# Kernel tuning notes

Hardware: AMD Instinct MI355X
Metric: run time of the kernel (lower is better)

## Reference

```python
import jax, jax.numpy as jnp
import numpy as np

NUM_HEADS = 16


def setup_inputs() -> dict:
    key = jax.random.key(0)
    ks = jax.random.split(key, 7)
    B_, N, C = 512, 64, 512
    x = jax.random.normal(ks[0], (B_, N, C), dtype=jnp.float32)
    attn_bias = jax.random.normal(ks[1], (NUM_HEADS, N, N), dtype=jnp.float32)
    mask = jax.random.normal(ks[2], (B_, N, N), dtype=jnp.float32)
    qkv_w = jax.random.normal(ks[3], (3 * C, C), dtype=jnp.float32) * (C ** -0.5)
    qkv_b = jax.random.normal(ks[4], (3 * C,), dtype=jnp.float32) * 0.02
    proj_w = jax.random.normal(ks[5], (C, C), dtype=jnp.float32) * (C ** -0.5)
    proj_b = jax.random.normal(ks[6], (C,), dtype=jnp.float32) * 0.02
    return {"x": x, "attn_bias": attn_bias, "mask": mask,
            "qkv_w": qkv_w, "qkv_b": qkv_b, "proj_w": proj_w, "proj_b": proj_b}


def reference(x, attn_bias, mask, qkv_w, qkv_b, proj_w, proj_b):
    B_, N, C = x.shape
    H = NUM_HEADS
    hd = C // H
    scale = hd ** -0.5
    # qkv projection: (B_, N, 3, H, hd) -> (3, B_, H, N, hd)
    qkv = (x @ qkv_w.T + qkv_b).reshape(B_, N, 3, H, hd)
    qkv = jnp.transpose(qkv, (2, 0, 3, 1, 4))
    q, k, v = qkv[0], qkv[1], qkv[2]
    attn = jnp.einsum('bhnd,bhmd->bhnm', q * scale, k)  # (B_, H, N, N)
    attn = attn + attn_bias            # (H, N, N) broadcasts over batch
    attn = attn + mask[:, None]        # (B_, 1, N, N)
    attn = jax.nn.softmax(attn, axis=-1)
    out = jnp.einsum('bhnm,bhmd->bhnd', attn, v)
    out = jnp.transpose(out, (0, 2, 1, 3)).reshape(B_, N, C)
    return out @ proj_w.T + proj_b
```

## Files before the change

kernel.cpp:

```cpp
#include <hip/hip_runtime.h>
#include <stdint.h>

typedef __attribute__((ext_vector_type(8))) __bf16 bf16x8;
typedef __attribute__((ext_vector_type(4))) float f32x4;
typedef __attribute__((ext_vector_type(4))) float fl4;
typedef __attribute__((ext_vector_type(8))) unsigned short us8;
typedef __attribute__((ext_vector_type(4))) unsigned short us4;

__device__ __forceinline__ unsigned short f2bf(float f) {
  union { float f; unsigned int u; } v;
  v.f = f;
  unsigned int r = v.u + 0x7FFFu + ((v.u >> 16) & 1u);
  return (unsigned short)(r >> 16);
}

#define GLOAD_LDS16(g, l)                                                   \
  __builtin_amdgcn_global_load_lds(                                         \
      (const __attribute__((address_space(1))) void*)(g),                   \
      (__attribute__((address_space(3))) void*)(l), 16, 0, 0)

__global__ void convert_all_kernel(const float* __restrict__ x,
                                   const float* __restrict__ wq,
                                   const float* __restrict__ wp,
                                   unsigned short* __restrict__ ox,
                                   unsigned short* __restrict__ owq,
                                   unsigned short* __restrict__ owp) {
  const int i = (blockIdx.x * blockDim.x + threadIdx.x) * 4;
  const float* src;
  unsigned short* dst;
  int off;
  if (i < 16777216) {
    src = x; dst = ox; off = i;
  } else if (i < 17563648) {
    src = wq; dst = owq; off = i - 16777216;
  } else {
    src = wp; dst = owp; off = i - 17563648;
  }
  fl4 v = *(const fl4*)(src + off);
  us4 o;
  o[0] = f2bf(v[0]);
  o[1] = f2bf(v[1]);
  o[2] = f2bf(v[2]);
  o[3] = f2bf(v[3]);
  *(us4*)(dst + off) = o;
}

template <bool OUT_BF16>
__global__ __launch_bounds__(512, 4) void gemm128_kernel(
    const unsigned short* __restrict__ A, const unsigned short* __restrict__ B,
    const float* __restrict__ bias, void* __restrict__ Cout, int M, int N,
    int K, int NT) {
  __shared__ __align__(16) unsigned short lds[32768];
  char* base = (char*)lds;

  const int tid = threadIdx.x;
  const int lane = tid & 63;
  const int wid = tid >> 6;
  const int lr = lane & 15;
  const int lg = lane >> 4;
  const int wm = wid >> 2;
  const int wn = wid & 3;

  const int bid = blockIdx.x;
  const int bm = ((bid & 31) + (bid / (32 * NT)) * 32) << 7;
  const int bn = (((bid >> 5) % NT)) << 7;

  const int srow = tid >> 3;
  const int scsw = ((tid & 7) << 4) ^ ((srow & 7) << 4);
  const char* Ag = (const char*)A;
  const char* Bg = (const char*)B;
  const size_t Kb = (size_t)K * 2;

#define STAGE(kt, p)                                                           \
  {                                                                            \
    char* la_ = base + (p)*32768;                                              \
    char* lb_ = la_ + 16384;                                                   \
    _Pragma("unroll") for (int i_ = 0; i_ < 2; ++i_) {                         \
      GLOAD_LDS16(Ag + (size_t)(bm + srow + i_ * 64) * Kb + (kt)*128 + scsw,   \
                  la_ + (srow + i_ * 64) * 128 + (tid & 7) * 16);              \
      GLOAD_LDS16(Bg + (size_t)(bn + srow + i_ * 64) * Kb + (kt)*128 + scsw,   \
                  lb_ + (srow + i_ * 64) * 128 + (tid & 7) * 16);              \
    }                                                                          \
  }

  const int swz = (lr & 7) << 4;
  const int ck0 = (lg << 4) ^ swz;
  const int ck1 = (64 + (lg << 4)) ^ swz;

  f32x4 acc[4][2];
#pragma unroll
  for (int m = 0; m < 4; ++m)
#pragma unroll
    for (int n = 0; n < 2; ++n) acc[m][n] = (f32x4){0.f, 0.f, 0.f, 0.f};

  const int nkt = K >> 6;

  STAGE(0, 0);
  __syncthreads();

  for (int kt = 0; kt < nkt; ++kt) {
    const int p = kt & 1;
    if (kt + 1 < nkt) STAGE(kt + 1, p ^ 1);

    const char* la = base + p * 32768;
    const char* lb = la + 16384;
    bf16x8 af[4][2], bfr[2][2];
#pragma unroll
    for (int m = 0; m < 4; ++m) {
      const int arow = (wm * 64 + m * 16 + lr) << 7;
      af[m][0] = *(const bf16x8*)(la + arow + ck0);
      af[m][1] = *(const bf16x8*)(la + arow + ck1);
    }
#pragma unroll
    for (int n = 0; n < 2; ++n) {
      const int brow = (wn * 32 + n * 16 + lr) << 7;
      bfr[n][0] = *(const bf16x8*)(lb + brow + ck0);
      bfr[n][1] = *(const bf16x8*)(lb + brow + ck1);
    }
#pragma unroll
    for (int kk = 0; kk < 2; ++kk)
#pragma unroll
      for (int m = 0; m < 4; ++m)
#pragma unroll
        for (int n = 0; n < 2; ++n)
          acc[m][n] = __builtin_amdgcn_mfma_f32_16x16x32_bf16(
              af[m][kk], bfr[n][kk], acc[m][n], 0, 0, 0);
    __syncthreads();
  }
#undef STAGE

  const int crow0 = bm + wm * 64 + lg * 4;
  const int ccol0 = bn + wn * 32 + lr;
#pragma unroll
  for (int n = 0; n < 2; ++n) {
    const int col = ccol0 + n * 16;
    const float bv = bias[col];
#pragma unroll
    for (int m = 0; m < 4; ++m) {
#pragma unroll
      for (int j = 0; j < 4; ++j) {
        const int row = crow0 + m * 16 + j;
        const float val = acc[m][n][j] + bv;
        if (OUT_BF16)
          ((unsigned short*)Cout)[(size_t)row * N + col] = f2bf(val);
        else
          ((float*)Cout)[(size_t)row * N + col] = val;
      }
    }
  }
}

__global__ __launch_bounds__(256, 4) void attn_kernel(
    const unsigned short* __restrict__ qkv, const float* __restrict__ abias,
    const float* __restrict__ mask, unsigned short* __restrict__ out) {
  __shared__ __align__(16) unsigned short lq[64 * 40];
  __shared__ __align__(16) unsigned short lk[64 * 40];
  __shared__ __align__(16) unsigned short lvT[32 * 72];
  __shared__ __align__(16) unsigned short lp[64 * 72];

  const int bid = blockIdx.x;
  const int id2 = (bid & 7) * 1024 + (bid >> 3);
  const int b = id2 >> 4;
  const int h = id2 & 15;
  const int tid = threadIdx.x;
  const int lane = tid & 63;
  const int wid = tid >> 6;
  const int lr = lane & 15;
  const int lg = lane >> 4;
  const int lk8 = lg * 8;

  {
    const int r = tid >> 2;
    const int d0 = (tid & 3) * 8;
    const size_t bse = (size_t)(b * 64 + r) * 1536 + h * 32 + d0;
    us8 qv = *(const us8*)(qkv + bse);
    us8 kv = *(const us8*)(qkv + bse + 512);
    us8 vv = *(const us8*)(qkv + bse + 1024);
    *(us8*)(lq + r * 40 + d0) = qv;
    *(us8*)(lk + r * 40 + d0) = kv;
#pragma unroll
    for (int i = 0; i < 8; ++i) lvT[(d0 + i) * 72 + r] = vv[i];
  }
  __syncthreads();

  f32x4 s[4];
  {
    bf16x8 aq = *(const bf16x8*)(lq + (wid * 16 + lr) * 40 + lk8);
#pragma unroll
    for (int n = 0; n < 4; ++n) {
      bf16x8 bk = *(const bf16x8*)(lk + (n * 16 + lr) * 40 + lk8);
      f32x4 z = {0.f, 0.f, 0.f, 0.f};
      s[n] = __builtin_amdgcn_mfma_f32_16x16x32_bf16(aq, bk, z, 0, 0, 0);
    }
  }
  const float scale = 0.17677669529663687f;
  const int row0 = wid * 16 + lg * 4;
#pragma unroll
  for (int j = 0; j < 4; ++j) {
    const int row = row0 + j;
    const float* ab = abias + (h * 64 + row) * 64 + lr;
    const float* mk = mask + ((size_t)b * 64 + row) * 64 + lr;
#pragma unroll
    for (int n = 0; n < 4; ++n)
      s[n][j] = s[n][j] * scale + ab[n * 16] + mk[n * 16];
  }

  float mx[4], sm[4];
#pragma unroll
  for (int j = 0; j < 4; ++j)
    mx[j] = fmaxf(fmaxf(s[0][j], s[1][j]), fmaxf(s[2][j], s[3][j]));
#pragma unroll
  for (int xm = 1; xm <= 8; xm <<= 1)
#pragma unroll
    for (int j = 0; j < 4; ++j) mx[j] = fmaxf(mx[j], __shfl_xor(mx[j], xm));
#pragma unroll
  for (int j = 0; j < 4; ++j) sm[j] = 0.f;
#pragma unroll
  for (int n = 0; n < 4; ++n)
#pragma unroll
    for (int j = 0; j < 4; ++j) {
      const float e = __expf(s[n][j] - mx[j]);
      s[n][j] = e;
      sm[j] += e;
    }
#pragma unroll
  for (int xm = 1; xm <= 8; xm <<= 1)
#pragma unroll
    for (int j = 0; j < 4; ++j) sm[j] += __shfl_xor(sm[j], xm);
#pragma unroll
  for (int j = 0; j < 4; ++j) sm[j] = 1.f / sm[j];
#pragma unroll
  for (int n = 0; n < 4; ++n)
#pragma unroll
    for (int j = 0; j < 4; ++j)
      lp[(row0 + j) * 72 + n * 16 + lr] = f2bf(s[n][j] * sm[j]);
  __syncthreads();

  f32x4 o[2];
  o[0] = (f32x4){0.f, 0.f, 0.f, 0.f};
  o[1] = o[0];
#pragma unroll
  for (int kk = 0; kk < 2; ++kk) {
    bf16x8 pa = *(const bf16x8*)(lp + (wid * 16 + lr) * 72 + kk * 32 + lk8);
#pragma unroll
    for (int d = 0; d < 2; ++d) {
      bf16x8 vb = *(const bf16x8*)(lvT + (d * 16 + lr) * 72 + kk * 32 + lk8);
      o[d] = __builtin_amdgcn_mfma_f32_16x16x32_bf16(pa, vb, o[d], 0, 0, 0);
    }
  }
#pragma unroll
  for (int d = 0; d < 2; ++d) {
    const int col = h * 32 + d * 16 + lr;
#pragma unroll
    for (int j = 0; j < 4; ++j) {
      const int row = row0 + j;
      out[(size_t)(b * 64 + row) * 512 + col] = f2bf(o[d][j]);
    }
  }
}

extern "C" void kernel_launch(void* const* d_in, const int* in_sizes, int n_in,
                              void* d_out, int out_size, void* d_ws,
                              size_t ws_size, hipStream_t stream) {
  (void)in_sizes; (void)n_in; (void)out_size; (void)ws_size;
  const float* x = (const float*)d_in[0];
  const float* abias = (const float*)d_in[1];
  const float* mask = (const float*)d_in[2];
  const float* qkv_w = (const float*)d_in[3];
  const float* qkv_b = (const float*)d_in[4];
  const float* proj_w = (const float*)d_in[5];
  const float* proj_b = (const float*)d_in[6];

  char* ws = (char*)d_ws;
  unsigned short* ws_x = (unsigned short*)(ws);
  unsigned short* ws_qkv = (unsigned short*)(ws + 33554432);
  unsigned short* ws_wq = (unsigned short*)(ws + 134217728);
  unsigned short* ws_wp = (unsigned short*)(ws + 135790592);
  unsigned short* ws_att = ws_x;

  convert_all_kernel<<<17408, 256, 0, stream>>>(x, qkv_w, proj_w, ws_x, ws_wq,
                                                ws_wp);

  gemm128_kernel<true><<<3072, 512, 0, stream>>>(ws_x, ws_wq, qkv_b, ws_qkv,
                                                 32768, 1536, 512, 12);

  attn_kernel<<<8192, 256, 0, stream>>>(ws_qkv, abias, mask, ws_att);

  gemm128_kernel<false><<<1024, 512, 0, stream>>>(ws_att, ws_wp, proj_b, d_out,
                                                  32768, 512, 512, 4);
}
```

Before: 259.9 us.

## Widen GEMM tiles to 128x256 with a triple-buffered async LDS pipeline

```diff
diff --git a/kernel.cpp b/kernel.cpp
--- a/kernel.cpp
+++ b/kernel.cpp
@@ -46,11 +46,11 @@
 }
 
 template <bool OUT_BF16>
-__global__ __launch_bounds__(512, 4) void gemm128_kernel(
+__global__ __launch_bounds__(512, 2) void gemm_k3_kernel(
     const unsigned short* __restrict__ A, const unsigned short* __restrict__ B,
     const float* __restrict__ bias, void* __restrict__ Cout, int M, int N,
     int K, int NT) {
-  __shared__ __align__(16) unsigned short lds[32768];
+  __shared__ __align__(16) unsigned short lds[73728];
   char* base = (char*)lds;
 
   const int tid = threadIdx.x;
@@ -63,7 +63,7 @@
 
   const int bid = blockIdx.x;
   const int bm = ((bid & 31) + (bid / (32 * NT)) * 32) << 7;
-  const int bn = (((bid >> 5) % NT)) << 7;
+  const int bn = ((bid >> 5) % NT) << 8;
 
   const int srow = tid >> 3;
   const int scsw = ((tid & 7) << 4) ^ ((srow & 7) << 4);
@@ -71,15 +71,17 @@
   const char* Bg = (const char*)B;
   const size_t Kb = (size_t)K * 2;
 
-#define STAGE(kt, p)                                                           \
+#define STAGE(kt)                                                              \
   {                                                                            \
-    char* la_ = base + (p)*32768;                                              \
+    char* la_ = base + ((kt) % 3) * 49152;                                     \
     char* lb_ = la_ + 16384;                                                   \
     _Pragma("unroll") for (int i_ = 0; i_ < 2; ++i_) {                         \
       GLOAD_LDS16(Ag + (size_t)(bm + srow + i_ * 64) * Kb + (kt)*128 + scsw,   \
-                  la_ + (srow + i_ * 64) * 128 + (tid & 7) * 16);              \
-      GLOAD_LDS16(Bg + (size_t)(bn + srow + i_ * 64) * Kb + (kt)*128 + scsw,   \
-                  lb_ + (srow + i_ * 64) * 128 + (tid & 7) * 16);              \
+                  la_ + (tid + i_ * 512) * 16);                                \
+    }                                                                          \
+    _Pragma("unroll") for (int j_ = 0; j_ < 4; ++j_) {                         \
+      GLOAD_LDS16(Bg + (size_t)(bn + srow + j_ * 64) * Kb + (kt)*128 + scsw,   \
+                  lb_ + (tid + j_ * 512) * 16);                                \
     }                                                                          \
   }
 
@@ -87,24 +89,29 @@
   const int ck0 = (lg << 4) ^ swz;
   const int ck1 = (64 + (lg << 4)) ^ swz;
 
-  f32x4 acc[4][2];
+  f32x4 acc[4][4];
 #pragma unroll
   for (int m = 0; m < 4; ++m)
 #pragma unroll
-    for (int n = 0; n < 2; ++n) acc[m][n] = (f32x4){0.f, 0.f, 0.f, 0.f};
+    for (int n = 0; n < 4; ++n) acc[m][n] = (f32x4){0.f, 0.f, 0.f, 0.f};
 
   const int nkt = K >> 6;
 
-  STAGE(0, 0);
-  __syncthreads();
+  STAGE(0);
+  STAGE(1);
 
   for (int kt = 0; kt < nkt; ++kt) {
-    const int p = kt & 1;
-    if (kt + 1 < nkt) STAGE(kt + 1, p ^ 1);
-
-    const char* la = base + p * 32768;
+    if (kt + 1 < nkt)
+      asm volatile("s_waitcnt vmcnt(6)" ::: "memory");
+    else
+      asm volatile("s_waitcnt vmcnt(0)" ::: "memory");
+    __builtin_amdgcn_s_barrier();
+    asm volatile("" ::: "memory");
+    if (kt + 2 < nkt) STAGE(kt + 2);
+
+    const char* la = base + (kt % 3) * 49152;
     const char* lb = la + 16384;
-    bf16x8 af[4][2], bfr[2][2];
+    bf16x8 af[4][2], bfr[4][2];
 #pragma unroll
     for (int m = 0; m < 4; ++m) {
       const int arow = (wm * 64 + m * 16 + lr) << 7;
@@ -112,8 +119,8 @@
       af[m][1] = *(const bf16x8*)(la + arow + ck1);
     }
 #pragma unroll
-    for (int n = 0; n < 2; ++n) {
-      const int brow = (wn * 32 + n * 16 + lr) << 7;
+    for (int n = 0; n < 4; ++n) {
+      const int brow = (wn * 64 + n * 16 + lr) << 7;
       bfr[n][0] = *(const bf16x8*)(lb + brow + ck0);
       bfr[n][1] = *(const bf16x8*)(lb + brow + ck1);
     }
@@ -122,17 +129,18 @@
 #pragma unroll
       for (int m = 0; m < 4; ++m)
 #pragma unroll
-        for (int n = 0; n < 2; ++n)
+        for (int n = 0; n < 4; ++n)
           acc[m][n] = __builtin_amdgcn_mfma_f32_16x16x32_bf16(
               af[m][kk], bfr[n][kk], acc[m][n], 0, 0, 0);
-    __syncthreads();
+    asm volatile("s_waitcnt lgkmcnt(0)" ::: "memory");
+    __builtin_amdgcn_sched_barrier(0);
   }
 #undef STAGE
 
   const int crow0 = bm + wm * 64 + lg * 4;
-  const int ccol0 = bn + wn * 32 + lr;
-#pragma unroll
-  for (int n = 0; n < 2; ++n) {
+  const int ccol0 = bn + wn * 64 + lr;
+#pragma unroll
+  for (int n = 0; n < 4; ++n) {
     const int col = ccol0 + n * 16;
     const float bv = bias[col];
 #pragma unroll
@@ -281,11 +289,11 @@
   convert_all_kernel<<<17408, 256, 0, stream>>>(x, qkv_w, proj_w, ws_x, ws_wq,
                                                 ws_wp);
 
-  gemm128_kernel<true><<<3072, 512, 0, stream>>>(ws_x, ws_wq, qkv_b, ws_qkv,
-                                                 32768, 1536, 512, 12);
+  gemm_k3_kernel<true><<<1536, 512, 0, stream>>>(ws_x, ws_wq, qkv_b, ws_qkv,
+                                                 32768, 1536, 512, 6);
 
   attn_kernel<<<8192, 256, 0, stream>>>(ws_qkv, abias, mask, ws_att);
 
-  gemm128_kernel<false><<<1024, 512, 0, stream>>>(ws_att, ws_wp, proj_b, d_out,
-                                                  32768, 512, 512, 4);
-}
+  gemm_k3_kernel<false><<<512, 512, 0, stream>>>(ws_att, ws_wp, proj_b, d_out,
+                                                 32768, 512, 512, 2);
+}
```

After: 268.5 us. +3.3%, slower.

## Process four heads per attention block with double-buffered prefetch; grid-stride bf16 conversion

Applied to the files above, without the earlier changes.

```diff
diff --git a/kernel.cpp b/kernel.cpp
--- a/kernel.cpp
+++ b/kernel.cpp
@@ -25,24 +25,27 @@
                                    unsigned short* __restrict__ ox,
                                    unsigned short* __restrict__ owq,
                                    unsigned short* __restrict__ owp) {
-  const int i = (blockIdx.x * blockDim.x + threadIdx.x) * 4;
-  const float* src;
-  unsigned short* dst;
-  int off;
-  if (i < 16777216) {
-    src = x; dst = ox; off = i;
-  } else if (i < 17563648) {
-    src = wq; dst = owq; off = i - 16777216;
-  } else {
-    src = wp; dst = owp; off = i - 17563648;
-  }
-  fl4 v = *(const fl4*)(src + off);
-  us4 o;
-  o[0] = f2bf(v[0]);
-  o[1] = f2bf(v[1]);
-  o[2] = f2bf(v[2]);
-  o[3] = f2bf(v[3]);
-  *(us4*)(dst + off) = o;
+  const int NCH = 2228224;
+  const int stride = gridDim.x * blockDim.x;
+  for (int c = blockIdx.x * blockDim.x + threadIdx.x; c < NCH; c += stride) {
+    const int i = c * 8;
+    const float* src;
+    unsigned short* dst;
+    int off;
+    if (i < 16777216) {
+      src = x; dst = ox; off = i;
+    } else if (i < 17563648) {
+      src = wq; dst = owq; off = i - 16777216;
+    } else {
+      src = wp; dst = owp; off = i - 17563648;
+    }
+    fl4 v0 = *(const fl4*)(src + off);
+    fl4 v1 = *(const fl4*)(src + off + 4);
+    us8 o;
+    o[0] = f2bf(v0[0]); o[1] = f2bf(v0[1]); o[2] = f2bf(v0[2]); o[3] = f2bf(v0[3]);
+    o[4] = f2bf(v1[0]); o[5] = f2bf(v1[1]); o[6] = f2bf(v1[2]); o[7] = f2bf(v1[3]);
+    *(us8*)(dst + off) = o;
+  }
 }
 
 template <bool OUT_BF16>
@@ -153,109 +156,136 @@
 __global__ __launch_bounds__(256, 4) void attn_kernel(
     const unsigned short* __restrict__ qkv, const float* __restrict__ abias,
     const float* __restrict__ mask, unsigned short* __restrict__ out) {
-  __shared__ __align__(16) unsigned short lq[64 * 40];
-  __shared__ __align__(16) unsigned short lk[64 * 40];
-  __shared__ __align__(16) unsigned short lvT[32 * 72];
+  __shared__ __align__(16) unsigned short bufs[2][7424];
   __shared__ __align__(16) unsigned short lp[64 * 72];
 
   const int bid = blockIdx.x;
-  const int id2 = (bid & 7) * 1024 + (bid >> 3);
-  const int b = id2 >> 4;
-  const int h = id2 & 15;
+  const int id2 = (bid & 7) * 256 + (bid >> 3);
+  const int b = id2 >> 2;
+  const int hq = (id2 & 3) << 2;
   const int tid = threadIdx.x;
   const int lane = tid & 63;
   const int wid = tid >> 6;
   const int lr = lane & 15;
   const int lg = lane >> 4;
   const int lk8 = lg * 8;
-
+  const int row0 = wid * 16 + lg * 4;
+  const float scale = 0.17677669529663687f;
+
+  const int sr = tid >> 2;
+  const int sd0 = (tid & 3) * 8;
+  const size_t sbase = (size_t)(b * 64 + sr) * 1536 + sd0;
+
+  us8 qv, kv, vv;
   {
-    const int r = tid >> 2;
-    const int d0 = (tid & 3) * 8;
-    const size_t bse = (size_t)(b * 64 + r) * 1536 + h * 32 + d0;
-    us8 qv = *(const us8*)(qkv + bse);
-    us8 kv = *(const us8*)(qkv + bse + 512);
-    us8 vv = *(const us8*)(qkv + bse + 1024);
-    *(us8*)(lq + r * 40 + d0) = qv;
-    *(us8*)(lk + r * 40 + d0) = kv;
-#pragma unroll
-    for (int i = 0; i < 8; ++i) lvT[(d0 + i) * 72 + r] = vv[i];
+    const unsigned short* p = qkv + sbase + hq * 32;
+    qv = *(const us8*)(p);
+    kv = *(const us8*)(p + 512);
+    vv = *(const us8*)(p + 1024);
+  }
+  {
+    unsigned short* d0b = bufs[0];
+    *(us8*)(d0b + sr * 40 + sd0) = qv;
+    *(us8*)(d0b + 2560 + sr * 40 + sd0) = kv;
+#pragma unroll
+    for (int i = 0; i < 8; ++i) d0b[5120 + (sd0 + i) * 72 + sr] = vv[i];
   }
   __syncthreads();
 
-  f32x4 s[4];
-  {
-    bf16x8 aq = *(const bf16x8*)(lq + (wid * 16 + lr) * 40 + lk8);
-#pragma unroll
-    for (int n = 0; n < 4; ++n) {
-      bf16x8 bk = *(const bf16x8*)(lk + (n * 16 + lr) * 40 + lk8);
-      f32x4 z = {0.f, 0.f, 0.f, 0.f};
-      s[n] = __builtin_amdgcn_mfma_f32_16x16x32_bf16(aq, bk, z, 0, 0, 0);
-    }
-  }
-  const float scale = 0.17677669529663687f;
-  const int row0 = wid * 16 + lg * 4;
-#pragma unroll
-  for (int j = 0; j < 4; ++j) {
-    const int row = row0 + j;
-    const float* ab = abias + (h * 64 + row) * 64 + lr;
-    const float* mk = mask + ((size_t)b * 64 + row) * 64 + lr;
-#pragma unroll
-    for (int n = 0; n < 4; ++n)
-      s[n][j] = s[n][j] * scale + ab[n * 16] + mk[n * 16];
-  }
-
-  float mx[4], sm[4];
-#pragma unroll
-  for (int j = 0; j < 4; ++j)
-    mx[j] = fmaxf(fmaxf(s[0][j], s[1][j]), fmaxf(s[2][j], s[3][j]));
-#pragma unroll
-  for (int xm = 1; xm <= 8; xm <<= 1)
-#pragma unroll
-    for (int j = 0; j < 4; ++j) mx[j] = fmaxf(mx[j], __shfl_xor(mx[j], xm));
-#pragma unroll
-  for (int j = 0; j < 4; ++j) sm[j] = 0.f;
-#pragma unroll
-  for (int n = 0; n < 4; ++n)
-#pragma unroll
-    for (int j = 0; j < 4; ++j) {
-      const float e = __expf(s[n][j] - mx[j]);
-      s[n][j] = e;
-      sm[j] += e;
-    }
-#pragma unroll
-  for (int xm = 1; xm <= 8; xm <<= 1)
-#pragma unroll
-    for (int j = 0; j < 4; ++j) sm[j] += __shfl_xor(sm[j], xm);
-#pragma unroll
-  for (int j = 0; j < 4; ++j) sm[j] = 1.f / sm[j];
-#pragma unroll
-  for (int n = 0; n < 4; ++n)
-#pragma unroll
-    for (int j = 0; j < 4; ++j)
-      lp[(row0 + j) * 72 + n * 16 + lr] = f2bf(s[n][j] * sm[j]);
-  __syncthreads();
-
-  f32x4 o[2];
-  o[0] = (f32x4){0.f, 0.f, 0.f, 0.f};
-  o[1] = o[0];
-#pragma unroll
-  for (int kk = 0; kk < 2; ++kk) {
-    bf16x8 pa = *(const bf16x8*)(lp + (wid * 16 + lr) * 72 + kk * 32 + lk8);
-#pragma unroll
-    for (int d = 0; d < 2; ++d) {
-      bf16x8 vb = *(const bf16x8*)(lvT + (d * 16 + lr) * 72 + kk * 32 + lk8);
-      o[d] = __builtin_amdgcn_mfma_f32_16x16x32_bf16(pa, vb, o[d], 0, 0, 0);
-    }
-  }
-#pragma unroll
-  for (int d = 0; d < 2; ++d) {
-    const int col = h * 32 + d * 16 + lr;
+#pragma unroll
+  for (int rr = 0; rr < 4; ++rr) {
+    const int h = hq + rr;
+    if (rr < 3) {
+      const unsigned short* p = qkv + sbase + (h + 1) * 32;
+      qv = *(const us8*)(p);
+      kv = *(const us8*)(p + 512);
+      vv = *(const us8*)(p + 1024);
+    }
+    const unsigned short* lq = bufs[rr & 1];
+    const unsigned short* lkk = lq + 2560;
+    const unsigned short* lvT = lq + 5120;
+
+    f32x4 s[4];
+    {
+      bf16x8 aq = *(const bf16x8*)(lq + (wid * 16 + lr) * 40 + lk8);
+#pragma unroll
+      for (int n = 0; n < 4; ++n) {
+        bf16x8 bk = *(const bf16x8*)(lkk + (n * 16 + lr) * 40 + lk8);
+        f32x4 z = {0.f, 0.f, 0.f, 0.f};
+        s[n] = __builtin_amdgcn_mfma_f32_16x16x32_bf16(aq, bk, z, 0, 0, 0);
+      }
+    }
 #pragma unroll
     for (int j = 0; j < 4; ++j) {
       const int row = row0 + j;
-      out[(size_t)(b * 64 + row) * 512 + col] = f2bf(o[d][j]);
-    }
+      const float* ab = abias + (h * 64 + row) * 64 + lr;
+      const float* mk = mask + ((size_t)b * 64 + row) * 64 + lr;
+#pragma unroll
+      for (int n = 0; n < 4; ++n)
+        s[n][j] = s[n][j] * scale + ab[n * 16] + mk[n * 16];
+    }
+
+    float mx[4], sm[4];
+#pragma unroll
+    for (int j = 0; j < 4; ++j)
+      mx[j] = fmaxf(fmaxf(s[0][j], s[1][j]), fmaxf(s[2][j], s[3][j]));
+#pragma unroll
+    for (int xm = 1; xm <= 8; xm <<= 1)
+#pragma unroll
+      for (int j = 0; j < 4; ++j) mx[j] = fmaxf(mx[j], __shfl_xor(mx[j], xm));
+#pragma unroll
+    for (int j = 0; j < 4; ++j) sm[j] = 0.f;
+#pragma unroll
+    for (int n = 0; n < 4; ++n)
+#pragma unroll
+      for (int j = 0; j < 4; ++j) {
+        const float e = __expf(s[n][j] - mx[j]);
+        s[n][j] = e;
+        sm[j] += e;
+      }
+#pragma unroll
+    for (int xm = 1; xm <= 8; xm <<= 1)
+#pragma unroll
+      for (int j = 0; j < 4; ++j) sm[j] += __shfl_xor(sm[j], xm);
+#pragma unroll
+    for (int j = 0; j < 4; ++j) sm[j] = 1.f / sm[j];
+#pragma unroll
+    for (int n = 0; n < 4; ++n)
+#pragma unroll
+      for (int j = 0; j < 4; ++j)
+        lp[(row0 + j) * 72 + n * 16 + lr] = f2bf(s[n][j] * sm[j]);
+    __syncthreads();
+
+    f32x4 o[2];
+    o[0] = (f32x4){0.f, 0.f, 0.f, 0.f};
+    o[1] = o[0];
+#pragma unroll
+    for (int kk = 0; kk < 2; ++kk) {
+      bf16x8 pa = *(const bf16x8*)(lp + (wid * 16 + lr) * 72 + kk * 32 + lk8);
+#pragma unroll
+      for (int d = 0; d < 2; ++d) {
+        bf16x8 vb = *(const bf16x8*)(lvT + (d * 16 + lr) * 72 + kk * 32 + lk8);
+        o[d] = __builtin_amdgcn_mfma_f32_16x16x32_bf16(pa, vb, o[d], 0, 0, 0);
+      }
+    }
+#pragma unroll
+    for (int d = 0; d < 2; ++d) {
+      const int col = h * 32 + d * 16 + lr;
+#pragma unroll
+      for (int j = 0; j < 4; ++j) {
+        const int row = row0 + j;
+        out[(size_t)(b * 64 + row) * 512 + col] = f2bf(o[d][j]);
+      }
+    }
+
+    if (rr < 3) {
+      unsigned short* db = bufs[(rr + 1) & 1];
+      *(us8*)(db + sr * 40 + sd0) = qv;
+      *(us8*)(db + 2560 + sr * 40 + sd0) = kv;
+#pragma unroll
+      for (int i = 0; i < 8; ++i) db[5120 + (sd0 + i) * 72 + sr] = vv[i];
+    }
+    __syncthreads();
   }
 }
 
@@ -278,13 +308,13 @@
   unsigned short* ws_wp = (unsigned short*)(ws + 135790592);
   unsigned short* ws_att = ws_x;
 
-  convert_all_kernel<<<17408, 256, 0, stream>>>(x, qkv_w, proj_w, ws_x, ws_wq,
-                                                ws_wp);
+  convert_all_kernel<<<2048, 256, 0, stream>>>(x, qkv_w, proj_w, ws_x, ws_wq,
+                                               ws_wp);
 
   gemm128_kernel<true><<<3072, 512, 0, stream>>>(ws_x, ws_wq, qkv_b, ws_qkv,
                                                  32768, 1536, 512, 12);
 
-  attn_kernel<<<8192, 256, 0, stream>>>(ws_qkv, abias, mask, ws_att);
+  attn_kernel<<<2048, 256, 0, stream>>>(ws_qkv, abias, mask, ws_att);
 
   gemm128_kernel<false><<<1024, 512, 0, stream>>>(ws_att, ws_wp, proj_b, d_out,
                                                   32768, 512, 512, 4);
```

Result: slower. 265.8 us (+2.3%).
